# Kernel optimization log

Measured on AMD Instinct MI355X. Metric: run time of the kernel, lower is better.

## Reference

```python
import jax, jax.numpy as jnp
import numpy as np

B, T, D, H, C = 128, 1000, 40, 128, 8  # batch, time, input feats, hidden, classes


def _lstm_layer(x, Wih, Whh, bih, bhh):
    """Unidirectional LSTM over time. x: [B,T,Din] -> [B,T,H]. PyTorch gate order i,f,g,o."""
    Bn = x.shape[0]
    Hn = Whh.shape[1]
    b = bih + bhh
    def step(carry, xt):
        h, c = carry
        g = xt @ Wih.T + h @ Whh.T + b  # [B,4H]
        i, f, gg, o = jnp.split(g, 4, axis=-1)
        c = jax.nn.sigmoid(f) * c + jax.nn.sigmoid(i) * jnp.tanh(gg)
        h = jax.nn.sigmoid(o) * jnp.tanh(c)
        return (h, c), h
    h0 = jnp.zeros((Bn, Hn), x.dtype)
    _, hs = jax.lax.scan(step, (h0, h0), jnp.swapaxes(x, 0, 1))  # scan over time
    return jnp.swapaxes(hs, 0, 1)


def _bilstm_layer(x, pf, pb):
    fwd = _lstm_layer(x, *pf)
    bwd = jnp.flip(_lstm_layer(jnp.flip(x, 1), *pb), 1)
    return jnp.concatenate([fwd, bwd], axis=-1)  # [B,T,2H]


def setup_inputs() -> dict:
    key = jax.random.key(0)
    ks = jax.random.split(key, 16)
    s = 0.05
    def rn(k, shape):
        return jax.random.normal(k, shape, jnp.float32) * s
    inp = {"x": jax.random.normal(ks[0], (B, T, D), jnp.float32)}
    inp["ln_g"] = jnp.ones((D,), jnp.float32)
    inp["ln_b"] = jnp.zeros((D,), jnp.float32)
    dims = [D, 2 * H]  # layer-0 input feats, layer-1 input feats
    i = 1
    for l in range(2):
        for d in ("f", "b"):
            inp[f"Wih_{d}{l}"] = rn(ks[i], (4 * H, dims[l])); i += 1
            inp[f"Whh_{d}{l}"] = rn(ks[i], (4 * H, H)); i += 1
            inp[f"bih_{d}{l}"] = jnp.zeros((4 * H,), jnp.float32)
            inp[f"bhh_{d}{l}"] = jnp.zeros((4 * H,), jnp.float32)
    inp["attn_W1"] = rn(ks[i], (H, 2 * H)); i += 1
    inp["attn_b1"] = jnp.zeros((H,), jnp.float32)
    inp["attn_w2"] = rn(ks[i], (1, H)); i += 1
    inp["fc_W1"] = rn(ks[i], (H, 2 * H)); i += 1
    inp["fc_b1"] = jnp.zeros((H,), jnp.float32)
    inp["fc_W2"] = rn(ks[i], (C, H)); i += 1
    inp["fc_b2"] = jnp.zeros((C,), jnp.float32)
    return inp


def reference(x, ln_g, ln_b,
              Wih_f0, Whh_f0, bih_f0, bhh_f0, Wih_b0, Whh_b0, bih_b0, bhh_b0,
              Wih_f1, Whh_f1, bih_f1, bhh_f1, Wih_b1, Whh_b1, bih_b1, bhh_b1,
              attn_W1, attn_b1, attn_w2, fc_W1, fc_b1, fc_W2, fc_b2):
    # LayerNorm over feature dim (eps=1e-5, PyTorch default)
    mu = jnp.mean(x, axis=-1, keepdims=True)
    var = jnp.var(x, axis=-1, keepdims=True)
    xn = (x - mu) * jax.lax.rsqrt(var + 1e-5) * ln_g + ln_b
    # 2-layer bidirectional LSTM
    h = _bilstm_layer(xn, (Wih_f0, Whh_f0, bih_f0, bhh_f0), (Wih_b0, Whh_b0, bih_b0, bhh_b0))
    h = _bilstm_layer(h, (Wih_f1, Whh_f1, bih_f1, bhh_f1), (Wih_b1, Whh_b1, bih_b1, bhh_b1))
    # attention pooling: Linear-Tanh-Linear(no bias) -> softmax over time
    scores = jnp.tanh(h @ attn_W1.T + attn_b1) @ attn_w2[0]  # [B,T]
    w = jax.nn.softmax(scores, axis=1)
    ctx = jnp.einsum('bt,btd->bd', w, h)  # [B,2H]
    # MLP classifier head
    hid = jax.nn.relu(ctx @ fc_W1.T + fc_b1)
    return hid @ fc_W2.T + fc_b2  # [B,C] logits
```

## Files before the change

kernel.cpp:

```cpp
#include <hip/hip_runtime.h>
#include <hip/hip_fp16.h>

#define T_ 1000

typedef float v2f __attribute__((ext_vector_type(2)));
typedef __fp16 h2t __attribute__((ext_vector_type(2)));

#if defined(__has_builtin)
#if __has_builtin(__builtin_amdgcn_fdot2)
#define HAS_FDOT2 1
#endif
#endif
#ifndef HAS_FDOT2
#define HAS_FDOT2 0
#endif

__device__ __forceinline__ float sigf(float x) { return 1.0f / (1.0f + __expf(-x)); }
__device__ __forceinline__ float tanh_fast(float x) { return 1.0f - 2.0f / (1.0f + __expf(2.0f * x)); }
__device__ __forceinline__ float dot4(float4 a, float4 b) {
  return a.x * b.x + a.y * b.y + a.z * b.z + a.w * b.w;
}
__device__ __forceinline__ void pkfma(v2f& acc, float4 w, float4 v) {
  v2f wl; wl[0] = w.x; wl[1] = w.y;
  v2f wh; wh[0] = w.z; wh[1] = w.w;
  v2f vl; vl[0] = v.x; vl[1] = v.y;
  v2f vh; vh[0] = v.z; vh[1] = v.w;
  acc += wl * vl;
  acc += wh * vh;
}
__device__ __forceinline__ unsigned short f2bf(float f) {
  unsigned u = __float_as_uint(f);
  u = (u + 0x7fffu + ((u >> 16) & 1u)) >> 16;
  return (unsigned short)u;
}
__device__ __forceinline__ float bf2f(unsigned short h) {
  return __uint_as_float(((unsigned)h) << 16);
}
__device__ __forceinline__ float4 bf4_to_f4(ushort4 u) {
  float4 r;
  r.x = bf2f(u.x); r.y = bf2f(u.y); r.z = bf2f(u.z); r.w = bf2f(u.w);
  return r;
}

__global__ void bail_kernel(float* out, int n) {
  for (int i = threadIdx.x; i < n; i += 256) out[i] = 0.0f;
}

__global__ __launch_bounds__(256) void ln_stats_kernel(const float* __restrict__ x,
                                                       float* __restrict__ mu_arr,
                                                       float* __restrict__ rs_arr) {
  const int lane = threadIdx.x & 63;
  const int w = threadIdx.x >> 6;
  const long row = (long)blockIdx.x * 4 + w;
  float v = (lane < 40) ? x[row * 40 + lane] : 0.0f;
  float s1 = v, s2 = v * v;
  for (int m = 32; m; m >>= 1) {
    s1 += __shfl_xor(s1, m, 64);
    s2 += __shfl_xor(s2, m, 64);
  }
  if (lane == 0) {
    const float mu = s1 * (1.0f / 40.0f);
    const float var = s2 * (1.0f / 40.0f) - mu * mu;
    mu_arr[row] = mu;
    rs_arr[row] = rsqrtf(var + 1e-5f);
  }
}

__global__ __launch_bounds__(256, 2) void gemm_xw0(
    const float* __restrict__ x,
    const float* __restrict__ mu_arr, const float* __restrict__ rs_arr,
    const float* __restrict__ ln_g, const float* __restrict__ ln_b,
    const float* __restrict__ Wf, const float* __restrict__ Wb,
    float* __restrict__ xwf, float* __restrict__ xwb,
    int Tc, int t0f, int t0b) {
  __shared__ float As[64 * 44];
  __shared__ float Bs[128 * 44];
  const int tid = threadIdx.x;
  const int tx = tid & 15, ty = tid >> 4;
  const int r0 = blockIdx.x * 64;
  const int jt = blockIdx.y;
  const int dir = jt >> 2, nh = jt & 3;
  const float* __restrict__ W = dir ? Wb : Wf;
  float* __restrict__ out = dir ? xwb : xwf;
  const int jbase = nh * 128;
  const int t0 = dir ? t0b : t0f;

  float4* As4 = (float4*)As;
  float4* Bs4 = (float4*)Bs;
  {
    const int row = tid >> 2;
    const int t4 = tid & 3;
    const int r = r0 + row;
    const int br = r / Tc;
    const long xrow = (long)br * T_ + t0 + (r - br * Tc);
    const float mu = mu_arr[xrow];
    const float rs = rs_arr[xrow];
#pragma unroll
    for (int m = 0; m < 3; ++m) {
      const int k4 = t4 + m * 4;
      if (k4 < 10) {
        const float4 v = *(const float4*)&x[xrow * 40 + k4 * 4];
        const float4 g4 = *(const float4*)&ln_g[k4 * 4];
        const float4 b4 = *(const float4*)&ln_b[k4 * 4];
        float4 xn;
        xn.x = (v.x - mu) * rs * g4.x + b4.x;
        xn.y = (v.y - mu) * rs * g4.y + b4.y;
        xn.z = (v.z - mu) * rs * g4.z + b4.z;
        xn.w = (v.w - mu) * rs * g4.w + b4.w;
        As4[row * 11 + k4] = xn;
      }
    }
  }
  {
    const int row = tid & 127;
    const int h = tid >> 7;
#pragma unroll
    for (int m = 0; m < 5; ++m) {
      const int k4 = h + m * 2;
      Bs4[row * 11 + k4] = *(const float4*)&W[(long)(jbase + row) * 40 + k4 * 4];
    }
  }
  __syncthreads();

  v2f acc2[4][8];
#pragma unroll
  for (int r = 0; r < 4; ++r)
#pragma unroll
    for (int c2 = 0; c2 < 8; ++c2) acc2[r][c2] = 0.0f;
#pragma unroll 1
  for (int k4 = 0; k4 < 10; ++k4) {
    float4 av[4];
#pragma unroll
    for (int r = 0; r < 4; ++r) av[r] = As4[(ty * 4 + r) * 11 + k4];
#pragma unroll
    for (int c2 = 0; c2 < 8; ++c2) {
      const float4 bv = Bs4[(tx + 16 * c2) * 11 + k4];
#pragma unroll
      for (int r = 0; r < 4; ++r) pkfma(acc2[r][c2], av[r], bv);
    }
  }
#pragma unroll
  for (int r = 0; r < 4; ++r) {
    const long ob = (long)(r0 + ty * 4 + r) * 512 + jbase + tx;
#pragma unroll
    for (int c2 = 0; c2 < 8; ++c2) out[ob + c2 * 16] = acc2[r][c2][0] + acc2[r][c2][1];
  }
}

__global__ __launch_bounds__(512) void rec_fused(
    const float* __restrict__ xw_f, const float* __restrict__ xw_b,
    const float* __restrict__ Whh_f, const float* __restrict__ Whh_b,
    const float* __restrict__ bih_f, const float* __restrict__ bhh_f,
    const float* __restrict__ bih_b, const float* __restrict__ bhh_b,
    float* __restrict__ h0out, unsigned short* __restrict__ h1out, int out_bf16,
    float* __restrict__ state, int Tc, int t0f, int t0b, int first) {
  const int tid = threadIdx.x;
  const int u = (tid >> 6) * 16 + ((tid & 63) >> 2);
  const int p = tid & 3;
  const int brow = blockIdx.x & 127;
  const int dir = blockIdx.x >> 7;
  const float* __restrict__ xw  = dir ? xw_b : xw_f;
  const float* __restrict__ Whh = dir ? Whh_b : Whh_f;
  const float* __restrict__ bih = dir ? bih_b : bih_f;
  const float* __restrict__ bhh = dir ? bhh_b : bhh_f;
  const int t0 = dir ? t0b : t0f;

  h2t whp[4][16];
#pragma unroll
  for (int g = 0; g < 4; ++g) {
    const float4* wr = (const float4*)(Whh + (g * 128 + u) * 128 + p * 32);
#pragma unroll
    for (int ff = 0; ff < 8; ++ff) {
      const float4 w4 = wr[(ff + 2 * p) & 7];
      h2t lo; lo[0] = (__fp16)w4.x; lo[1] = (__fp16)w4.y;
      h2t hi; hi[0] = (__fp16)w4.z; hi[1] = (__fp16)w4.w;
      whp[g][2 * ff] = lo;
      whp[g][2 * ff + 1] = hi;
    }
  }
  const int myrow = p * 128 + u;
  const float bias_p = bih[myrow] + bhh[myrow];

  __shared__ float h4f[2][128];
  __shared__ float hring[2][8][128];
  float* sblk = state + (long)blockIdx.x * 256;
  float c = 0.0f;
  if (first) {
    if (tid < 128) h4f[0][tid] = 0.0f;
  } else {
    if (tid < 128) h4f[0][tid] = sblk[tid];
    c = sblk[128 + u];
  }
  const long gbase = (long)brow * Tc;
  float xr[8];
#pragma unroll
  for (int v = 0; v < 8; ++v) {
    xr[v] = 0.0f;
    if (v < Tc) {
      const int tr = dir ? (Tc - 1 - v) : v;
      xr[v] = xw[(gbase + tr) * 512 + myrow];
    }
  }
  __syncthreads();

  const int nSB = (Tc + 7) / 8;
  const long obase = (long)brow * T_;
  for (int sb = 0; sb < nSB; ++sb) {
    const int rb = sb & 1;
#pragma unroll
    for (int su = 0; su < 8; ++su) {
      const int s = sb * 8 + su;
      if (s >= Tc) break;
      const int rdq = su & 1, wrq = rdq ^ 1;
      if (su == 0 && sb > 0) {
#pragma unroll
        for (int e = 0; e < 2; ++e) {
          const int idx = tid + e * 512;
          const int v = idx >> 7, j = idx & 127;
          const int s2 = (sb - 1) * 8 + v;
          const int tt = dir ? (Tc - 1 - s2) : s2;
          const long oidx = (obase + (t0 + tt)) * 256 + dir * 128 + j;
          const float hval = hring[rb ^ 1][v][j];
          if (out_bf16) h1out[oidx] = f2bf(hval);
          else          h0out[oidx] = hval;
        }
      }
      float a0 = 0.f, a1 = 0.f, a2 = 0.f, a3 = 0.f;
      const float4* h4v = (const float4*)h4f[rdq];
#pragma unroll
      for (int ff = 0; ff < 8; ++ff) {
        const float4 hv = h4v[p * 8 + ((ff + 2 * p) & 7)];
#if HAS_FDOT2
        const h2t hp0 = __builtin_amdgcn_cvt_pkrtz(hv.x, hv.y);
        const h2t hp1 = __builtin_amdgcn_cvt_pkrtz(hv.z, hv.w);
        a0 = __builtin_amdgcn_fdot2(hp0, whp[0][2 * ff], a0, false);
        a0 = __builtin_amdgcn_fdot2(hp1, whp[0][2 * ff + 1], a0, false);
        a1 = __builtin_amdgcn_fdot2(hp0, whp[1][2 * ff], a1, false);
        a1 = __builtin_amdgcn_fdot2(hp1, whp[1][2 * ff + 1], a1, false);
        a2 = __builtin_amdgcn_fdot2(hp0, whp[2][2 * ff], a2, false);
        a2 = __builtin_amdgcn_fdot2(hp1, whp[2][2 * ff + 1], a2, false);
        a3 = __builtin_amdgcn_fdot2(hp0, whp[3][2 * ff], a3, false);
        a3 = __builtin_amdgcn_fdot2(hp1, whp[3][2 * ff + 1], a3, false);
#else
        a0 = fmaf((float)whp[0][2 * ff][0], hv.x, a0);
        a0 = fmaf((float)whp[0][2 * ff][1], hv.y, a0);
        a0 = fmaf((float)whp[0][2 * ff + 1][0], hv.z, a0);
        a0 = fmaf((float)whp[0][2 * ff + 1][1], hv.w, a0);
        a1 = fmaf((float)whp[1][2 * ff][0], hv.x, a1);
        a1 = fmaf((float)whp[1][2 * ff][1], hv.y, a1);
        a1 = fmaf((float)whp[1][2 * ff + 1][0], hv.z, a1);
        a1 = fmaf((float)whp[1][2 * ff + 1][1], hv.w, a1);
        a2 = fmaf((float)whp[2][2 * ff][0], hv.x, a2);
        a2 = fmaf((float)whp[2][2 * ff][1], hv.y, a2);
        a2 = fmaf((float)whp[2][2 * ff + 1][0], hv.z, a2);
        a2 = fmaf((float)whp[2][2 * ff + 1][1], hv.w, a2);
        a3 = fmaf((float)whp[3][2 * ff][0], hv.x, a3);
        a3 = fmaf((float)whp[3][2 * ff][1], hv.y, a3);
        a3 = fmaf((float)whp[3][2 * ff + 1][0], hv.z, a3);
        a3 = fmaf((float)whp[3][2 * ff + 1][1], hv.w, a3);
#endif
      }
      const float xin = xr[su] + bias_p;
      float pg0 = a0 + ((p == 0) ? xin : 0.0f);
      float pg1 = a1 + ((p == 1) ? xin : 0.0f);
      float pg2 = a2 + ((p == 2) ? xin : 0.0f);
      float pg3 = a3 + ((p == 3) ? xin : 0.0f);
      pg0 += __shfl_xor(pg0, 1, 64); pg0 += __shfl_xor(pg0, 2, 64);
      pg1 += __shfl_xor(pg1, 1, 64); pg1 += __shfl_xor(pg1, 2, 64);
      pg2 += __shfl_xor(pg2, 1, 64); pg2 += __shfl_xor(pg2, 2, 64);
      pg3 += __shfl_xor(pg3, 1, 64); pg3 += __shfl_xor(pg3, 2, 64);
      const float ig = sigf(pg0);
      const float fg = sigf(pg1);
      const float gg = tanh_fast(pg2);
      const float og = sigf(pg3);
      c = fg * c + ig * gg;
      const float hv2 = og * tanh_fast(c);
      if (p == 0) { h4f[wrq][u] = hv2; hring[rb][su][u] = hv2; }
      if (su == 7) {
#pragma unroll
        for (int v = 0; v < 8; ++v) {
          const int sn = s + 1 + v;
          xr[v] = 0.0f;
          if (sn < Tc) {
            const int tr = dir ? (Tc - 1 - sn) : sn;
            xr[v] = xw[(gbase + tr) * 512 + myrow];
          }
        }
      }
      __syncthreads();
    }
  }
  {
    const int sbL = (Tc - 1) >> 3;
    const int cnt = Tc - sbL * 8;
    const int rbL = sbL & 1;
#pragma unroll
    for (int e = 0; e < 2; ++e) {
      const int idx = tid + e * 512;
      const int v = idx >> 7, j = idx & 127;
      if (v < cnt) {
        const int s2 = sbL * 8 + v;
        const int tt = dir ? (Tc - 1 - s2) : s2;
        const long oidx = (obase + (t0 + tt)) * 256 + dir * 128 + j;
        const float hval = hring[rbL][v][j];
        if (out_bf16) h1out[oidx] = f2bf(hval);
        else          h0out[oidx] = hval;
      }
    }
  }
  if (tid < 128) sblk[tid] = h4f[Tc & 1][tid];
  if (p == 0) sblk[128 + u] = c;
}

__global__ __launch_bounds__(256, 2) void gemm_xw1(
    const float* __restrict__ h0,
    const float* __restrict__ Wf, const float* __restrict__ Wb,
    float* __restrict__ xwf, float* __restrict__ xwb,
    int Tc, int t0f, int t0b) {
  __shared__ float As[64 * 36];
  __shared__ float Bs[128 * 36];
  __shared__ int rowbase[64];
  const int tid = threadIdx.x;
  const int tx = tid & 15, ty = tid >> 4;
  const int r0 = blockIdx.x * 64;
  const int jt = blockIdx.y;
  const int dir = jt >> 2;
  const int nh = jt & 3;
  const float* __restrict__ W = dir ? Wb : Wf;
  float* __restrict__ out = dir ? xwb : xwf;
  const int jbase = nh * 128;
  const int t0 = dir ? t0b : t0f;

  if (tid < 64) {
    const int r = r0 + tid;
    const int br = r / Tc;
    rowbase[tid] = br * T_ + t0 + (r - br * Tc);
  }

  float4* As4 = (float4*)As;
  float4* Bs4 = (float4*)Bs;
  v2f acc2[4][8];
#pragma unroll
  for (int r = 0; r < 4; ++r)
#pragma unroll
    for (int c2 = 0; c2 < 8; ++c2) acc2[r][c2] = 0.0f;
#pragma unroll 1
  for (int kk = 0; kk < 8; ++kk) {
    __syncthreads();
#pragma unroll
    for (int i = 0; i < 2; ++i) {
      const int q = tid + i * 256;
      const int row = q >> 3, k4 = q & 7;
      As4[row * 9 + k4] = *(const float4*)&h0[(long)rowbase[row] * 256 + kk * 32 + k4 * 4];
    }
#pragma unroll
    for (int i = 0; i < 4; ++i) {
      const int q = tid + i * 256;
      const int row = q >> 3, k4 = q & 7;
      Bs4[row * 9 + k4] = *(const float4*)&W[(long)(jbase + row) * 256 + kk * 32 + k4 * 4];
    }
    __syncthreads();
#pragma unroll 1
    for (int k4 = 0; k4 < 8; ++k4) {
      float4 av[4];
#pragma unroll
      for (int r = 0; r < 4; ++r) av[r] = As4[(ty * 4 + r) * 9 + k4];
#pragma unroll
      for (int c2 = 0; c2 < 8; ++c2) {
        const float4 bv = Bs4[(tx + 16 * c2) * 9 + k4];
#pragma unroll
        for (int r = 0; r < 4; ++r) pkfma(acc2[r][c2], av[r], bv);
      }
    }
  }
#pragma unroll
  for (int r = 0; r < 4; ++r) {
    const long ob = (long)(r0 + ty * 4 + r) * 512 + jbase + tx;
#pragma unroll
    for (int c2 = 0; c2 < 8; ++c2) out[ob + c2 * 16] = acc2[r][c2][0] + acc2[r][c2][1];
  }
}

__global__ __launch_bounds__(256, 2) void score_kernel(
    const unsigned short* __restrict__ h1b, const float* __restrict__ W1,
    const float* __restrict__ b1, const float* __restrict__ w2,
    float* __restrict__ scores) {
  __shared__ float As[64 * 36];
  __shared__ float Bs[128 * 36];
  const int tid = threadIdx.x;
  const int tx = tid & 15, ty = tid >> 4;
  const long r0 = (long)blockIdx.x * 64;

  float4* As4 = (float4*)As;
  float4* Bs4 = (float4*)Bs;
  v2f acc2[4][8];
#pragma unroll
  for (int r = 0; r < 4; ++r)
#pragma unroll
    for (int c2 = 0; c2 < 8; ++c2) acc2[r][c2] = 0.0f;
#pragma unroll 1
  for (int kk = 0; kk < 8; ++kk) {
    __syncthreads();
#pragma unroll
    for (int i = 0; i < 2; ++i) {
      const int q = tid + i * 256;
      const int row = q >> 3, k4 = q & 7;
      const ushort4 uv = *(const ushort4*)&h1b[(r0 + row) * 256 + kk * 32 + k4 * 4];
      As4[row * 9 + k4] = bf4_to_f4(uv);
    }
#pragma unroll
    for (int i = 0; i < 4; ++i) {
      const int q = tid + i * 256;
      const int row = q >> 3, k4 = q & 7;
      Bs4[row * 9 + k4] = *(const float4*)&W1[(long)row * 256 + kk * 32 + k4 * 4];
    }
    __syncthreads();
#pragma unroll 1
    for (int k4 = 0; k4 < 8; ++k4) {
      float4 av[4];
#pragma unroll
      for (int r = 0; r < 4; ++r) av[r] = As4[(ty * 4 + r) * 9 + k4];
#pragma unroll
      for (int c2 = 0; c2 < 8; ++c2) {
        const float4 bv = Bs4[(tx + 16 * c2) * 9 + k4];
#pragma unroll
        for (int r = 0; r < 4; ++r) pkfma(acc2[r][c2], av[r], bv);
      }
    }
  }
#pragma unroll
  for (int r = 0; r < 4; ++r) {
    float s = 0.0f;
#pragma unroll
    for (int c2 = 0; c2 < 8; ++c2) {
      const int col = tx + 16 * c2;
      s += tanh_fast(acc2[r][c2][0] + acc2[r][c2][1] + b1[col]) * w2[col];
    }
#pragma unroll
    for (int m = 1; m < 16; m <<= 1) s += __shfl_xor(s, m, 16);
    if (tx == 0) scores[r0 + ty * 4 + r] = s;
  }
}

__global__ __launch_bounds__(256, 2) void head_kernel(
    const float* __restrict__ scores, const unsigned short* __restrict__ h1b,
    const float* __restrict__ fW1, const float* __restrict__ fb1,
    const float* __restrict__ fW2, const float* __restrict__ fb2,
    float* __restrict__ outp) {
  const int b = blockIdx.x, tid = threadIdx.x;
  __shared__ float wls[1000];
  __shared__ float red[8];
  __shared__ __align__(16) float ctx[256];
  __shared__ __align__(16) float hid[128];

  float sv[4];
  float mx = -1e30f;
#pragma unroll
  for (int i = 0; i < 4; ++i) {
    const int t = tid + i * 256;
    sv[i] = (t < 1000) ? scores[b * 1000 + t] : -1e30f;
    mx = fmaxf(mx, sv[i]);
  }
  for (int m = 32; m; m >>= 1) mx = fmaxf(mx, __shfl_xor(mx, m, 64));
  if ((tid & 63) == 0) red[tid >> 6] = mx;
  __syncthreads();
  mx = fmaxf(fmaxf(red[0], red[1]), fmaxf(red[2], red[3]));
  float se = 0.0f;
#pragma unroll
  for (int i = 0; i < 4; ++i) {
    const int t = tid + i * 256;
    if (t < 1000) {
      const float e = __expf(sv[i] - mx);
      wls[t] = e;
      se += e;
    }
  }
  for (int m = 32; m; m >>= 1) se += __shfl_xor(se, m, 64);
  if ((tid & 63) == 0) red[4 + (tid >> 6)] = se;
  __syncthreads();
  const float rinv = 1.0f / (red[4] + red[5] + red[6] + red[7]);

  float a = 0.0f;
  const unsigned short* hb = h1b + (long)b * T_ * 256 + tid;
  for (int t = 0; t < T_; ++t) a = fmaf(wls[t], bf2f(hb[t * 256]), a);
  ctx[tid] = a * rinv;
  __syncthreads();
  if (tid < 128) {
    float s = fb1[tid];
    const float4* wr = (const float4*)&fW1[tid * 256];
    const float4* cc = (const float4*)ctx;
#pragma unroll
    for (int f = 0; f < 64; ++f) s += dot4(wr[f], cc[f]);
    hid[tid] = fmaxf(s, 0.0f);
  }
  __syncthreads();
  if (tid < 8) {
    float s = fb2[tid];
    const float4* wr = (const float4*)&fW2[tid * 128];
    const float4* hh = (const float4*)hid;
#pragma unroll
    for (int f = 0; f < 32; ++f) s += dot4(wr[f], hh[f]);
    outp[b * 8 + tid] = s;
  }
}

extern "C" void kernel_launch(void* const* d_in, const int* in_sizes, int n_in,
                              void* d_out, int out_size, void* d_ws, size_t ws_size,
                              hipStream_t stream) {
  (void)in_sizes; (void)n_in; (void)out_size;
  const float* x       = (const float*)d_in[0];
  const float* ln_g    = (const float*)d_in[1];
  const float* ln_b    = (const float*)d_in[2];
  const float* Wih_f0  = (const float*)d_in[3];
  const float* Whh_f0  = (const float*)d_in[4];
  const float* bih_f0  = (const float*)d_in[5];
  const float* bhh_f0  = (const float*)d_in[6];
  const float* Wih_b0  = (const float*)d_in[7];
  const float* Whh_b0  = (const float*)d_in[8];
  const float* bih_b0  = (const float*)d_in[9];
  const float* bhh_b0  = (const float*)d_in[10];
  const float* Wih_f1  = (const float*)d_in[11];
  const float* Whh_f1  = (const float*)d_in[12];
  const float* bih_f1  = (const float*)d_in[13];
  const float* bhh_f1  = (const float*)d_in[14];
  const float* Wih_b1  = (const float*)d_in[15];
  const float* Whh_b1  = (const float*)d_in[16];
  const float* bih_b1  = (const float*)d_in[17];
  const float* bhh_b1  = (const float*)d_in[18];
  const float* attn_W1 = (const float*)d_in[19];
  const float* attn_b1 = (const float*)d_in[20];
  const float* attn_w2 = (const float*)d_in[21];
  const float* fc_W1   = (const float*)d_in[22];
  const float* fc_b1   = (const float*)d_in[23];
  const float* fc_W2   = (const float*)d_in[24];
  const float* fc_b2   = (const float*)d_in[25];

  char* base = (char*)d_ws;
  size_t off = 0;
  auto alloc = [&](size_t bytes) {
    char* ptr = base + off;
    off += (bytes + 255) & ~(size_t)255;
    return ptr;
  };
  float*          h0    = (float*)alloc(32768000ull * 4);
  unsigned short* h1b   = (unsigned short*)alloc(32768000ull * 2);
  float*          state = (float*)alloc(65536ull * 4);
  float*          scor  = (float*)alloc(128000ull * 4);
  float*          mu_a  = (float*)alloc(128000ull * 4);
  float*          rs_a  = (float*)alloc(128000ull * 4);

  const size_t rem = (ws_size > off) ? (ws_size - off) : 0;
  static const int cands[16] = {1000, 500, 250, 200, 125, 100, 50, 40, 25, 20, 10, 8, 5, 4, 2, 1};
  int Tc = 0;
  for (int ci = 0; ci < 16; ++ci) {
    if (524288ull * (size_t)cands[ci] <= rem) { Tc = cands[ci]; break; }
  }
  if (Tc == 0) {
    bail_kernel<<<dim3(1), dim3(256), 0, stream>>>((float*)d_out, 1024);
    return;
  }
  float* xwf = (float*)(base + off);
  float* xwb = xwf + 65536L * Tc;

  ln_stats_kernel<<<dim3(32000), dim3(256), 0, stream>>>(x, mu_a, rs_a);
  const int nch = T_ / Tc;
  for (int ch = 0; ch < nch; ++ch) {
    const int t0f = ch * Tc;
    const int t0b = T_ - (ch + 1) * Tc;
    gemm_xw0<<<dim3(2 * Tc, 8), dim3(256), 0, stream>>>(x, mu_a, rs_a, ln_g, ln_b,
                                                        Wih_f0, Wih_b0, xwf, xwb, Tc, t0f, t0b);
    rec_fused<<<dim3(256), dim3(512), 0, stream>>>(xwf, xwb, Whh_f0, Whh_b0,
                                                   bih_f0, bhh_f0, bih_b0, bhh_b0,
                                                   h0, h1b, 0, state, Tc, t0f, t0b,
                                                   (ch == 0) ? 1 : 0);
  }
  for (int ch = 0; ch < nch; ++ch) {
    const int t0f = ch * Tc;
    const int t0b = T_ - (ch + 1) * Tc;
    gemm_xw1<<<dim3(2 * Tc, 8), dim3(256), 0, stream>>>(h0, Wih_f1, Wih_b1, xwf, xwb, Tc, t0f, t0b);
    rec_fused<<<dim3(256), dim3(512), 0, stream>>>(xwf, xwb, Whh_f1, Whh_b1,
                                                   bih_f1, bhh_f1, bih_b1, bhh_b1,
                                                   h0, h1b, 1, state, Tc, t0f, t0b,
                                                   (ch == 0) ? 1 : 0);
  }
  score_kernel<<<dim3(2000), dim3(256), 0, stream>>>(h1b, attn_W1, attn_b1, attn_w2, scor);
  head_kernel<<<dim3(128), dim3(256), 0, stream>>>(scor, h1b, fc_W1, fc_b1, fc_W2, fc_b2,
                                                   (float*)d_out);
}
```

Before: 3.220 ms.

## Store input projections and shared hidden state in fp16, lighten recurrence barrier

The precomputed input-gate projections are now written and read as fp16, which halves their memory traffic and workspace size and so allows larger time chunks. The recurrent hidden state in shared memory is kept as packed fp16, so each thread reads 8 halves per LDS load and no longer converts to fp16 every step. __syncthreads is replaced by an inline s_waitcnt lgkmcnt(0) plus s_barrier, and the final hidden state is saved from a register. This costs some accuracy from fp16 rounding of the projections and the hidden state. The custom barrier waits only on LDS and scalar-memory counters, not on vector memory operations.

```diff
diff --git a/kernel.cpp b/kernel.cpp
--- a/kernel.cpp
+++ b/kernel.cpp
@@ -5,6 +5,7 @@
 
 typedef float v2f __attribute__((ext_vector_type(2)));
 typedef __fp16 h2t __attribute__((ext_vector_type(2)));
+typedef __fp16 h8v_t __attribute__((ext_vector_type(8)));
 
 #if defined(__has_builtin)
 #if __has_builtin(__builtin_amdgcn_fdot2)
@@ -14,6 +15,8 @@
 #ifndef HAS_FDOT2
 #define HAS_FDOT2 0
 #endif
+
+#define REC_BARRIER() asm volatile("s_waitcnt lgkmcnt(0)\n\ts_barrier" ::: "memory")
 
 __device__ __forceinline__ float sigf(float x) { return 1.0f / (1.0f + __expf(-x)); }
 __device__ __forceinline__ float tanh_fast(float x) { return 1.0f - 2.0f / (1.0f + __expf(2.0f * x)); }
@@ -71,7 +74,7 @@
     const float* __restrict__ mu_arr, const float* __restrict__ rs_arr,
     const float* __restrict__ ln_g, const float* __restrict__ ln_b,
     const float* __restrict__ Wf, const float* __restrict__ Wb,
-    float* __restrict__ xwf, float* __restrict__ xwb,
+    __fp16* __restrict__ xwf, __fp16* __restrict__ xwb,
     int Tc, int t0f, int t0b) {
   __shared__ float As[64 * 44];
   __shared__ float Bs[128 * 44];
@@ -81,7 +84,7 @@
   const int jt = blockIdx.y;
   const int dir = jt >> 2, nh = jt & 3;
   const float* __restrict__ W = dir ? Wb : Wf;
-  float* __restrict__ out = dir ? xwb : xwf;
+  __fp16* __restrict__ out = dir ? xwb : xwf;
   const int jbase = nh * 128;
   const int t0 = dir ? t0b : t0f;
 
@@ -143,12 +146,12 @@
   for (int r = 0; r < 4; ++r) {
     const long ob = (long)(r0 + ty * 4 + r) * 512 + jbase + tx;
 #pragma unroll
-    for (int c2 = 0; c2 < 8; ++c2) out[ob + c2 * 16] = acc2[r][c2][0] + acc2[r][c2][1];
+    for (int c2 = 0; c2 < 8; ++c2) out[ob + c2 * 16] = (__fp16)(acc2[r][c2][0] + acc2[r][c2][1]);
   }
 }
 
 __global__ __launch_bounds__(512) void rec_fused(
-    const float* __restrict__ xw_f, const float* __restrict__ xw_b,
+    const __fp16* __restrict__ xw_f, const __fp16* __restrict__ xw_b,
     const float* __restrict__ Whh_f, const float* __restrict__ Whh_b,
     const float* __restrict__ bih_f, const float* __restrict__ bhh_f,
     const float* __restrict__ bih_b, const float* __restrict__ bhh_b,
@@ -159,7 +162,7 @@
   const int p = tid & 3;
   const int brow = blockIdx.x & 127;
   const int dir = blockIdx.x >> 7;
-  const float* __restrict__ xw  = dir ? xw_b : xw_f;
+  const __fp16* __restrict__ xw = dir ? xw_b : xw_f;
   const float* __restrict__ Whh = dir ? Whh_b : Whh_f;
   const float* __restrict__ bih = dir ? bih_b : bih_f;
   const float* __restrict__ bhh = dir ? bhh_b : bhh_f;
@@ -168,27 +171,36 @@
   h2t whp[4][16];
 #pragma unroll
   for (int g = 0; g < 4; ++g) {
-    const float4* wr = (const float4*)(Whh + (g * 128 + u) * 128 + p * 32);
-#pragma unroll
-    for (int ff = 0; ff < 8; ++ff) {
-      const float4 w4 = wr[(ff + 2 * p) & 7];
-      h2t lo; lo[0] = (__fp16)w4.x; lo[1] = (__fp16)w4.y;
-      h2t hi; hi[0] = (__fp16)w4.z; hi[1] = (__fp16)w4.w;
-      whp[g][2 * ff] = lo;
-      whp[g][2 * ff + 1] = hi;
+    const float4* wr4 = (const float4*)(Whh + (g * 128 + u) * 128);
+#pragma unroll
+    for (int ff = 0; ff < 4; ++ff) {
+      const int c4 = (ff + p) & 3;
+      const float4 wa = wr4[p * 8 + c4 * 2];
+      const float4 wb = wr4[p * 8 + c4 * 2 + 1];
+      h2t t0v; t0v[0] = (__fp16)wa.x; t0v[1] = (__fp16)wa.y;
+      h2t t1v; t1v[0] = (__fp16)wa.z; t1v[1] = (__fp16)wa.w;
+      h2t t2v; t2v[0] = (__fp16)wb.x; t2v[1] = (__fp16)wb.y;
+      h2t t3v; t3v[0] = (__fp16)wb.z; t3v[1] = (__fp16)wb.w;
+      whp[g][ff * 4 + 0] = t0v;
+      whp[g][ff * 4 + 1] = t1v;
+      whp[g][ff * 4 + 2] = t2v;
+      whp[g][ff * 4 + 3] = t3v;
     }
   }
   const int myrow = p * 128 + u;
   const float bias_p = bih[myrow] + bhh[myrow];
 
-  __shared__ float h4f[2][128];
+  __shared__ h2t h16[2][64];
   __shared__ float hring[2][8][128];
   float* sblk = state + (long)blockIdx.x * 256;
-  float c = 0.0f;
+  float c = 0.0f, hlast = 0.0f;
   if (first) {
-    if (tid < 128) h4f[0][tid] = 0.0f;
+    if (tid < 64) { h2t z; z[0] = (__fp16)0.0f; z[1] = (__fp16)0.0f; h16[0][tid] = z; }
   } else {
-    if (tid < 128) h4f[0][tid] = sblk[tid];
+    if (tid < 64) {
+      h2t pr; pr[0] = (__fp16)sblk[2 * tid]; pr[1] = (__fp16)sblk[2 * tid + 1];
+      h16[0][tid] = pr;
+    }
     c = sblk[128 + u];
   }
   const long gbase = (long)brow * Tc;
@@ -198,7 +210,7 @@
     xr[v] = 0.0f;
     if (v < Tc) {
       const int tr = dir ? (Tc - 1 - v) : v;
-      xr[v] = xw[(gbase + tr) * 512 + myrow];
+      xr[v] = (float)xw[(gbase + tr) * 512 + myrow];
     }
   }
   __syncthreads();
@@ -226,38 +238,45 @@
         }
       }
       float a0 = 0.f, a1 = 0.f, a2 = 0.f, a3 = 0.f;
-      const float4* h4v = (const float4*)h4f[rdq];
-#pragma unroll
-      for (int ff = 0; ff < 8; ++ff) {
-        const float4 hv = h4v[p * 8 + ((ff + 2 * p) & 7)];
+      const h8v_t* hp = (const h8v_t*)h16[rdq];
+#pragma unroll
+      for (int ff = 0; ff < 4; ++ff) {
+        const int c4 = (ff + p) & 3;
+        const h8v_t hx = hp[p * 4 + c4];
+        const h2t x0 = __builtin_shufflevector(hx, hx, 0, 1);
+        const h2t x1 = __builtin_shufflevector(hx, hx, 2, 3);
+        const h2t x2 = __builtin_shufflevector(hx, hx, 4, 5);
+        const h2t x3 = __builtin_shufflevector(hx, hx, 6, 7);
 #if HAS_FDOT2
-        const h2t hp0 = __builtin_amdgcn_cvt_pkrtz(hv.x, hv.y);
-        const h2t hp1 = __builtin_amdgcn_cvt_pkrtz(hv.z, hv.w);
-        a0 = __builtin_amdgcn_fdot2(hp0, whp[0][2 * ff], a0, false);
-        a0 = __builtin_amdgcn_fdot2(hp1, whp[0][2 * ff + 1], a0, false);
-        a1 = __builtin_amdgcn_fdot2(hp0, whp[1][2 * ff], a1, false);
-        a1 = __builtin_amdgcn_fdot2(hp1, whp[1][2 * ff + 1], a1, false);
-        a2 = __builtin_amdgcn_fdot2(hp0, whp[2][2 * ff], a2, false);
-        a2 = __builtin_amdgcn_fdot2(hp1, whp[2][2 * ff + 1], a2, false);
-        a3 = __builtin_amdgcn_fdot2(hp0, whp[3][2 * ff], a3, false);
-        a3 = __builtin_amdgcn_fdot2(hp1, whp[3][2 * ff + 1], a3, false);
+        a0 = __builtin_amdgcn_fdot2(x0, whp[0][ff * 4 + 0], a0, false);
+        a0 = __builtin_amdgcn_fdot2(x1, whp[0][ff * 4 + 1], a0, false);
+        a0 = __builtin_amdgcn_fdot2(x2, whp[0][ff * 4 + 2], a0, false);
+        a0 = __builtin_amdgcn_fdot2(x3, whp[0][ff * 4 + 3], a0, false);
+        a1 = __builtin_amdgcn_fdot2(x0, whp[1][ff * 4 + 0], a1, false);
+        a1 = __builtin_amdgcn_fdot2(x1, whp[1][ff * 4 + 1], a1, false);
+        a1 = __builtin_amdgcn_fdot2(x2, whp[1][ff * 4 + 2], a1, false);
+        a1 = __builtin_amdgcn_fdot2(x3, whp[1][ff * 4 + 3], a1, false);
+        a2 = __builtin_amdgcn_fdot2(x0, whp[2][ff * 4 + 0], a2, false);
+        a2 = __builtin_amdgcn_fdot2(x1, whp[2][ff * 4 + 1], a2, false);
+        a2 = __builtin_amdgcn_fdot2(x2, whp[2][ff * 4 + 2], a2, false);
+        a2 = __builtin_amdgcn_fdot2(x3, whp[2][ff * 4 + 3], a2, false);
+        a3 = __builtin_amdgcn_fdot2(x0, whp[3][ff * 4 + 0], a3, false);
+        a3 = __builtin_amdgcn_fdot2(x1, whp[3][ff * 4 + 1], a3, false);
+        a3 = __builtin_amdgcn_fdot2(x2, whp[3][ff * 4 + 2], a3, false);
+        a3 = __builtin_amdgcn_fdot2(x3, whp[3][ff * 4 + 3], a3, false);
 #else
-        a0 = fmaf((float)whp[0][2 * ff][0], hv.x, a0);
-        a0 = fmaf((float)whp[0][2 * ff][1], hv.y, a0);
-        a0 = fmaf((float)whp[0][2 * ff + 1][0], hv.z, a0);
-        a0 = fmaf((float)whp[0][2 * ff + 1][1], hv.w, a0);
-        a1 = fmaf((float)whp[1][2 * ff][0], hv.x, a1);
-        a1 = fmaf((float)whp[1][2 * ff][1], hv.y, a1);
-        a1 = fmaf((float)whp[1][2 * ff + 1][0], hv.z, a1);
-        a1 = fmaf((float)whp[1][2 * ff + 1][1], hv.w, a1);
-        a2 = fmaf((float)whp[2][2 * ff][0], hv.x, a2);
-        a2 = fmaf((float)whp[2][2 * ff][1], hv.y, a2);
-        a2 = fmaf((float)whp[2][2 * ff + 1][0], hv.z, a2);
-        a2 = fmaf((float)whp[2][2 * ff + 1][1], hv.w, a2);
-        a3 = fmaf((float)whp[3][2 * ff][0], hv.x, a3);
-        a3 = fmaf((float)whp[3][2 * ff][1], hv.y, a3);
-        a3 = fmaf((float)whp[3][2 * ff + 1][0], hv.z, a3);
-        a3 = fmaf((float)whp[3][2 * ff + 1][1], hv.w, a3);
+        const h2t xs[4] = {x0, x1, x2, x3};
+#pragma unroll
+        for (int j = 0; j < 4; ++j) {
+          a0 = fmaf((float)xs[j][0], (float)whp[0][ff * 4 + j][0], a0);
+          a0 = fmaf((float)xs[j][1], (float)whp[0][ff * 4 + j][1], a0);
+          a1 = fmaf((float)xs[j][0], (float)whp[1][ff * 4 + j][0], a1);
+          a1 = fmaf((float)xs[j][1], (float)whp[1][ff * 4 + j][1], a1);
+          a2 = fmaf((float)xs[j][0], (float)whp[2][ff * 4 + j][0], a2);
+          a2 = fmaf((float)xs[j][1], (float)whp[2][ff * 4 + j][1], a2);
+          a3 = fmaf((float)xs[j][0], (float)whp[3][ff * 4 + j][0], a3);
+          a3 = fmaf((float)xs[j][1], (float)whp[3][ff * 4 + j][1], a3);
+        }
 #endif
       }
       const float xin = xr[su] + bias_p;
@@ -275,7 +294,11 @@
       const float og = sigf(pg3);
       c = fg * c + ig * gg;
       const float hv2 = og * tanh_fast(c);
-      if (p == 0) { h4f[wrq][u] = hv2; hring[rb][su][u] = hv2; }
+      if (p == 0) {
+        ((__fp16*)h16[wrq])[u] = (__fp16)hv2;
+        hring[rb][su][u] = hv2;
+        hlast = hv2;
+      }
       if (su == 7) {
 #pragma unroll
         for (int v = 0; v < 8; ++v) {
@@ -283,11 +306,11 @@
           xr[v] = 0.0f;
           if (sn < Tc) {
             const int tr = dir ? (Tc - 1 - sn) : sn;
-            xr[v] = xw[(gbase + tr) * 512 + myrow];
+            xr[v] = (float)xw[(gbase + tr) * 512 + myrow];
           }
         }
       }
-      __syncthreads();
+      REC_BARRIER();
     }
   }
   {
@@ -308,14 +331,13 @@
       }
     }
   }
-  if (tid < 128) sblk[tid] = h4f[Tc & 1][tid];
-  if (p == 0) sblk[128 + u] = c;
+  if (p == 0) { sblk[u] = hlast; sblk[128 + u] = c; }
 }
 
 __global__ __launch_bounds__(256, 2) void gemm_xw1(
     const float* __restrict__ h0,
     const float* __restrict__ Wf, const float* __restrict__ Wb,
-    float* __restrict__ xwf, float* __restrict__ xwb,
+    __fp16* __restrict__ xwf, __fp16* __restrict__ xwb,
     int Tc, int t0f, int t0b) {
   __shared__ float As[64 * 36];
   __shared__ float Bs[128 * 36];
@@ -327,7 +349,7 @@
   const int dir = jt >> 2;
   const int nh = jt & 3;
   const float* __restrict__ W = dir ? Wb : Wf;
-  float* __restrict__ out = dir ? xwb : xwf;
+  __fp16* __restrict__ out = dir ? xwb : xwf;
   const int jbase = nh * 128;
   const int t0 = dir ? t0b : t0f;
 
@@ -377,7 +399,7 @@
   for (int r = 0; r < 4; ++r) {
     const long ob = (long)(r0 + ty * 4 + r) * 512 + jbase + tx;
 #pragma unroll
-    for (int c2 = 0; c2 < 8; ++c2) out[ob + c2 * 16] = acc2[r][c2][0] + acc2[r][c2][1];
+    for (int c2 = 0; c2 < 8; ++c2) out[ob + c2 * 16] = (__fp16)(acc2[r][c2][0] + acc2[r][c2][1]);
   }
 }
 
@@ -553,14 +575,14 @@
   static const int cands[16] = {1000, 500, 250, 200, 125, 100, 50, 40, 25, 20, 10, 8, 5, 4, 2, 1};
   int Tc = 0;
   for (int ci = 0; ci < 16; ++ci) {
-    if (524288ull * (size_t)cands[ci] <= rem) { Tc = cands[ci]; break; }
+    if (262144ull * (size_t)cands[ci] <= rem) { Tc = cands[ci]; break; }
   }
   if (Tc == 0) {
     bail_kernel<<<dim3(1), dim3(256), 0, stream>>>((float*)d_out, 1024);
     return;
   }
-  float* xwf = (float*)(base + off);
-  float* xwb = xwf + 65536L * Tc;
+  __fp16* xwf = (__fp16*)(base + off);
+  __fp16* xwb = xwf + 65536L * Tc;
 
   ln_stats_kernel<<<dim3(32000), dim3(256), 0, stream>>>(x, mu_a, rs_a);
   const int nch = T_ / Tc;
```

Measured after the change: 3.380 ms. 1.05x slower.
